# Optimization experiments

Measured on AMD Instinct MI355X. Metric: run time of the kernel, lower is better.

The kernel has to match this reference:

```python
import jax, jax.numpy as jnp
import numpy as np

N_RAYS = 8192
N_SAMPLES = 64   # timesteps per ray
HID = 128
BOOSTER = 1.0
FAR = 10.0


def rsh_cart_3(d):
    # real spherical harmonics, cartesian, degree 3 -> 16 coefficients
    x, y, z = d[..., 0], d[..., 1], d[..., 2]
    x2, y2, z2 = x * x, y * y, z * z
    return jnp.stack([
        jnp.full_like(x, 0.282094791773878),
        -0.488602511902920 * y,
        0.488602511902920 * z,
        -0.488602511902920 * x,
        1.092548430592079 * x * y,
        -1.092548430592079 * y * z,
        0.315391565252520 * (3.0 * z2 - 1.0),
        -1.092548430592079 * x * z,
        0.546274215296040 * (x2 - y2),
        -0.590043589926644 * y * (3.0 * x2 - y2),
        2.890611442640554 * x * y * z,
        -0.457045799464466 * y * (5.0 * z2 - 1.0),
        0.373176332590115 * z * (5.0 * z2 - 3.0),
        -0.457045799464466 * x * (5.0 * z2 - 1.0),
        1.445305721320277 * z * (x2 - y2),
        -0.590043589926644 * x * (x2 - 3.0 * y2),
    ], axis=-1)


def setup_inputs() -> dict:
    key = jax.random.key(0)
    ks = jax.random.split(key, 10)
    N, H = N_RAYS, HID

    def w(k, shape, fan_in):
        return (jax.random.normal(k, shape, jnp.float32) / np.float32(np.sqrt(fan_in)))

    return dict(
        rays_o=jax.random.normal(ks[0], (N, 3), jnp.float32) * 0.3,
        rays_d=jax.random.normal(ks[1], (N, 3), jnp.float32),
        aabb=jnp.array([[-1.0, -1.0, -1.0], [1.0, 1.0, 1.0]], jnp.float32),
        W1=w(ks[2], (3, H), 3), b1=jnp.zeros((H,), jnp.float32),
        W2=w(ks[3], (H, H), H), b2=jnp.zeros((H,), jnp.float32),
        Wd=w(ks[4], (H, 1), H), bd=jnp.zeros((1,), jnp.float32),
        Wf=w(ks[5], (H, 16), H), bf=jnp.zeros((16,), jnp.float32),
        Wc1=w(ks[6], (32, H), 32), bc1=jnp.zeros((H,), jnp.float32),
        Wc2=w(ks[7], (H, 3), H), bc2=jnp.zeros((3,), jnp.float32),
    )


def reference(rays_o, rays_d, aabb, W1, b1, W2, b2, Wd, bd, Wf, bf, Wc1, bc1, Wc2, bc2):
    # --- ray / AABB intersection (slab test), as in RayBundle.intersect_aabb ---
    inv_d = 1.0 / rays_d
    t1 = (aabb[0] - rays_o) * inv_d
    t2 = (aabb[1] - rays_o) * inv_d
    tnear = jnp.maximum(jnp.max(jnp.minimum(t1, t2), -1), 0.0)      # (N,)
    tfar = jnp.minimum(jnp.min(jnp.maximum(t1, t2), -1), FAR)       # (N,)
    active = tnear < tfar                                           # active_mask()
    tnear = jnp.where(active, tnear, 0.0)
    tfar = jnp.where(active, tfar, 1.0)

    # --- timestep sampler: midpoint stratification between tnear/tfar ---
    T = N_SAMPLES
    frac = (jnp.arange(T, dtype=rays_o.dtype) + 0.5) / T
    ts = tnear[:, None] + frac[None, :] * (tfar - tnear)[:, None]    # (N,T)
    xyz = rays_o[:, None, :] + rays_d[:, None, :] * ts[..., None]    # (N,T,3)

    # --- convert_world_to_box_normalized + BoundsFilter.test ---
    xyz_ndc = (xyz - aabb[0]) / (aabb[1] - aabb[0]) * 2.0 - 1.0
    inside = jnp.all((xyz_ndc >= -1.0) & (xyz_ndc <= 1.0), -1)       # (N,T)

    # --- direction harmonics (rsh_cart_3 of normalized direction) ---
    dnorm = jnp.linalg.norm(rays_d, axis=-1, keepdims=True)          # (N,1)
    ynm = rsh_cart_3(rays_d / dnorm)                                 # (N,16)

    # --- radiance field MLP (query-everywhere; masked points contribute 0) ---
    h = jax.nn.relu(xyz_ndc @ W1 + b1)
    h = jax.nn.relu(h @ W2 + b2)
    sigma = jnp.exp(h @ Wd + bd)[..., 0]                             # (N,T) density
    feat = h @ Wf + bf                                               # (N,T,16)
    cond = jnp.broadcast_to(ynm[:, None, :], feat.shape)
    hc = jax.nn.relu(jnp.concatenate([feat, cond], -1) @ Wc1 + bc1)
    color = jax.nn.sigmoid(hc @ Wc2 + bc2)                           # (N,T,3)
    m = inside.astype(sigma.dtype)
    sigma = sigma * m                                                # scatter-zeros equiv
    color = color * m[..., None]

    # --- integrate_timesteps: transmittance * alpha weights ---
    tfinal = tfar + BOOSTER
    deltas = jnp.concatenate([ts[:, 1:] - ts[:, :-1], tfinal[:, None] - ts[:, -1:]], -1)
    tau = sigma * deltas * dnorm                                     # (N,T)
    excl = jnp.concatenate([jnp.zeros_like(tau[:, :1]), jnp.cumsum(tau[:, :-1], -1)], -1)
    weights = jnp.exp(-excl) * (1.0 - jnp.exp(-tau))                 # (N,T)

    # --- color_map / alpha_map / depth_map ---
    cmap = jnp.einsum('nt,ntc->nc', weights, color)                  # (N,3)
    amap = jnp.sum(weights, -1, keepdims=True)                       # (N,1)
    dmap = jnp.sum(weights * ts, -1, keepdims=True)                  # (N,1)
    am = active[:, None].astype(cmap.dtype)
    return jnp.concatenate([cmap * am, amap * am, dmap * am], -1)    # (N,5)
```

## Files before the change

kernel.cpp:

```cpp
#include <hip/hip_runtime.h>
#include <math.h>

#define THREADS 512
#define GRID 512
#define NRAYS 8192
#define FAR_T 10.0f
#define CSTR 24

typedef __attribute__((ext_vector_type(8))) short short8;
typedef __attribute__((ext_vector_type(4))) float f32x4;

static __device__ __forceinline__ unsigned f2bfu(float f) {
    unsigned u = __builtin_bit_cast(unsigned, f);
    return (u + 0x7fffu + ((u >> 16) & 1u)) >> 16;
}
static __device__ __forceinline__ unsigned pk2(float a, float b) {
    unsigned ra = __builtin_bit_cast(unsigned, a) + 0x8000u;
    unsigned rb = __builtin_bit_cast(unsigned, b) + 0x8000u;
    return __builtin_amdgcn_perm(rb, ra, 0x07060302u);
}
static __device__ __forceinline__ int sw128(int r, int k) { return (r << 7) + (k ^ ((r & 7) << 3)); }
static __device__ __forceinline__ int sw32(int r, int k)  { return (r << 5) + (k ^ ((r & 3) << 3)); }
static __device__ __forceinline__ f32x4 MFMA16(short8 a, short8 b, f32x4 c) {
    return __builtin_amdgcn_mfma_f32_16x16x32_bf16(a, b, c, 0, 0, 0);
}

struct RayP { float ox,oy,oz,dx,dy,dz,tn,tf,tstep,dnorm; bool act; };

static __device__ __forceinline__ RayP raySetup(const float* __restrict__ ro, const float* __restrict__ rd,
        int r, float a0x,float a0y,float a0z,float a1x,float a1y,float a1z) {
    RayP R;
    R.ox=ro[3*r+0]; R.oy=ro[3*r+1]; R.oz=ro[3*r+2];
    R.dx=rd[3*r+0]; R.dy=rd[3*r+1]; R.dz=rd[3*r+2];
    float ivx=1.f/R.dx, ivy=1.f/R.dy, ivz=1.f/R.dz;
    float t1x=(a0x-R.ox)*ivx, t2x=(a1x-R.ox)*ivx;
    float t1y=(a0y-R.oy)*ivy, t2y=(a1y-R.oy)*ivy;
    float t1z=(a0z-R.oz)*ivz, t2z=(a1z-R.oz)*ivz;
    float tn = fmaxf(fmaxf(fminf(t1x,t2x),fminf(t1y,t2y)),fminf(t1z,t2z));
    tn = fmaxf(tn, 0.f);
    float tf = fminf(fminf(fmaxf(t1x,t2x),fmaxf(t1y,t2y)),fmaxf(t1z,t2z));
    tf = fminf(tf, FAR_T);
    R.act = tn < tf;
    R.tn = R.act ? tn : 0.f;
    R.tf = R.act ? tf : 1.f;
    R.tstep = (R.tf - R.tn) * (1.f/64.f);
    R.dnorm = sqrtf(R.dx*R.dx + R.dy*R.dy + R.dz*R.dz);
    return R;
}

__global__ __launch_bounds__(THREADS, 4)
void RadianceRenderer_kernel(const float* __restrict__ rays_o, const float* __restrict__ rays_d,
                             const float* __restrict__ aabb,
                             const float* __restrict__ W1, const float* __restrict__ b1,
                             const float* __restrict__ W2, const float* __restrict__ b2,
                             const float* __restrict__ Wd, const float* __restrict__ bd,
                             const float* __restrict__ Wf, const float* __restrict__ bf,
                             const float* __restrict__ Wc1, const float* __restrict__ bc1,
                             const float* __restrict__ Wc2, const float* __restrict__ bc2,
                             float* __restrict__ out)
{
    __shared__ __align__(16) short W1T[128*8];
    __shared__ __align__(16) short Wfd17[17*128];
    __shared__ __align__(16) short Wc2T3[3*128];
    __shared__ __align__(16) float B2F[128];
    __shared__ __align__(16) float BC1F[128];
    __shared__ __align__(16) union {
        struct { short W2T[128*128]; short Wc1T[128*32]; } w;
        struct { short H1[128*128]; short H2[128*128];
                 short CC[128*CSTR];
                 float CS[4*128]; } a;
    } sm;

    const int tid  = threadIdx.x;
    const int lane = tid & 63;
    const int wv   = tid >> 6;
    const int l15  = lane & 15;
    const int l4   = lane >> 4;
    const short8 z8 = {0,0,0,0,0,0,0,0};

    for (int i = tid; i < 128*128; i += THREADS) {
        int k = i >> 7, n = i & 127;
        sm.w.W2T[sw128(n, k)] = (short)f2bfu(W2[i]);
    }
    for (int i = tid; i < 128*32; i += THREADS) {
        int n = i >> 5, k = i & 31;
        sm.w.Wc1T[sw32(n, k)] = (short)f2bfu(Wc1[k*128 + n]);
    }
    for (int i = tid; i < 17*128; i += THREADS) {
        int n = i >> 7, k = i & 127;
        float v = (n < 16) ? Wf[k*16 + n] : Wd[k];
        Wfd17[sw128(n, k)] = (short)f2bfu(v);
    }
    for (int i = tid; i < 3*128; i += THREADS) {
        int c = i >> 7, k = i & 127;
        Wc2T3[i] = (short)f2bfu(Wc2[k*3 + c]);
    }
    for (int i = tid; i < 128*8; i += THREADS) {
        int ch = i >> 3, k = i & 7;
        float f = (k < 3) ? W1[k*128 + ch] : ((k == 3) ? b1[ch] : 0.f);
        W1T[i] = (short)f2bfu(f);
    }
    for (int i = tid; i < 128; i += THREADS) { B2F[i] = b2[i]; BC1F[i] = bc1[i]; }
    __syncthreads();

    const int chB = (wv >> 1) * 32;
    const int smB = (wv & 1) * 64;
    const int sB3 = wv * 16;

    short8 w2f[2][4], wc1f[2];
    #pragma unroll
    for (int jn = 0; jn < 2; ++jn)
        #pragma unroll
        for (int kk = 0; kk < 4; ++kk)
            w2f[jn][kk] = *(const short8*)&sm.w.W2T[sw128(chB + 16*jn + l15, kk*32 + 8*l4)];
    #pragma unroll
    for (int cg = 0; cg < 2; ++cg)
        wc1f[cg] = *(const short8*)&sm.w.Wc1T[sw32(chB + 16*cg + l15, 8*l4)];

    f32x4 bfv;
    #pragma unroll
    for (int vv = 0; vv < 4; ++vv) bfv[vv] = bf[4*l4 + vv];
    float bc2r[3] = { bc2[0], bc2[1], bc2[2] };
    const float bdr = bd[0];

    const float a0x=aabb[0],a0y=aabb[1],a0z=aabb[2],a1x=aabb[3],a1y=aabb[4],a1z=aabb[5];
    const float scx=2.f/(a1x-a0x), scy=2.f/(a1y-a0y), scz=2.f/(a1z-a0z);

    __syncthreads();

    for (int i = tid; i < 128*CSTR/2; i += THREADS) ((unsigned*)sm.a.CC)[i] = 0u;
    __syncthreads();

    int gp = -1;

    for (int g = blockIdx.x; g < NRAYS/2; g += gridDim.x) {
        if (wv == 4 || wv == 5) {
            const int m   = tid - 256;
            const int ray = 2*g + (m >> 6);
            RayP R = raySetup(rays_o, rays_d, ray, a0x,a0y,a0z,a1x,a1y,a1z);
            const int s = m & 63;
            float t  = R.tn + ((float)s + 0.5f) * R.tstep;
            float px = fmaf(R.dx, t, R.ox);
            float py = fmaf(R.dy, t, R.oy);
            float pz = fmaf(R.dz, t, R.oz);
            float nx = fmaf(px - a0x, scx, -1.f);
            float ny = fmaf(py - a0y, scy, -1.f);
            float nz = fmaf(pz - a0z, scz, -1.f);
            *(uint2*)&sm.a.CC[m*CSTR] = make_uint2(pk2(nx, ny), pk2(nz, 1.0f));
            if (s == 0) {
                float inorm = 1.f / R.dnorm;
                float x = R.dx*inorm, y = R.dy*inorm, z = R.dz*inorm;
                float x2 = x*x, y2 = y*y, z2 = z*z;
                unsigned q0 = pk2(0.282094791773878f,              -0.488602511902920f*y);
                unsigned q1 = pk2(0.488602511902920f*z,            -0.488602511902920f*x);
                unsigned q2 = pk2(1.092548430592079f*x*y,          -1.092548430592079f*y*z);
                unsigned q3 = pk2(0.315391565252520f*(3.f*z2-1.f), -1.092548430592079f*x*z);
                unsigned q4 = pk2(0.546274215296040f*(x2-y2),      -0.590043589926644f*y*(3.f*x2-y2));
                unsigned q5 = pk2(2.890611442640554f*x*y*z,        -0.457045799464466f*y*(5.f*z2-1.f));
                unsigned q6 = pk2(0.373176332590115f*z*(5.f*z2-3.f), -0.457045799464466f*x*(5.f*z2-1.f));
                unsigned q7 = pk2(1.445305721320277f*z*(x2-y2),    -0.590043589926644f*x*(x2-3.f*y2));
                *(uint4*)&sm.a.CC[m*CSTR + 16]        = make_uint4(q0,q1,q2,q3);
                *(uint4*)&sm.a.CC[(m+1)*CSTR + 16]    = make_uint4(q4,q5,q6,q7);
            }
        } else if (wv < 2 && gp >= 0) {
            RayP R = raySetup(rays_o, rays_d, 2*gp + wv, a0x,a0y,a0z,a1x,a1y,a1z);
            const int m = wv*64 + lane;
            float t  = R.tn + ((float)lane + 0.5f) * R.tstep;
            float px = fmaf(R.dx, t, R.ox);
            float py = fmaf(R.dy, t, R.oy);
            float pz = fmaf(R.dz, t, R.oz);
            float nx = fmaf(px - a0x, scx, -1.f);
            float ny = fmaf(py - a0y, scy, -1.f);
            float nz = fmaf(pz - a0z, scz, -1.f);
            bool ins = (nx >= -1.f) & (nx <= 1.f) & (ny >= -1.f) & (ny <= 1.f)
                     & (nz >= -1.f) & (nz <= 1.f);
            float sig = ins ? __expf(sm.a.CS[3*128 + m] + bdr) : 0.f;
            float delta = (lane == 63) ? (R.tf + 1.0f - t) : R.tstep;
            float tau = sig * delta * R.dnorm;
            float cum = tau;
            #pragma unroll
            for (int off = 1; off < 64; off <<= 1) {
                float tmp = __shfl_up(cum, off);
                if (lane >= off) cum += tmp;
            }
            float excl = cum - tau;
            float wgt = __expf(-excl) * (1.f - __expf(-tau));
            float c0 = wgt * sm.a.CS[0*128 + m];
            float c1 = wgt * sm.a.CS[1*128 + m];
            float c2 = wgt * sm.a.CS[2*128 + m];
            float amv = wgt;
            float dmv = wgt * t;
            #pragma unroll
            for (int off = 32; off; off >>= 1) {
                c0  += __shfl_xor(c0,  off);
                c1  += __shfl_xor(c1,  off);
                c2  += __shfl_xor(c2,  off);
                amv += __shfl_xor(amv, off);
                dmv += __shfl_xor(dmv, off);
            }
            if (lane == 0) {
                float msk = R.act ? 1.f : 0.f;
                int ray = 2*gp + wv;
                out[ray*5+0] = c0*msk;
                out[ray*5+1] = c1*msk;
                out[ray*5+2] = c2*msk;
                out[ray*5+3] = amv*msk;
                out[ray*5+4] = dmv*msk;
            }
        }
        __syncthreads();

        {
            short8 bx[4];
            #pragma unroll
            for (int im = 0; im < 4; ++im) {
                short8 v = z8;
                if (l4 == 0) v = *(const short8*)&sm.a.CC[(smB + 16*im + l15)*CSTR];
                bx[im] = v;
            }
            #pragma unroll
            for (int jn = 0; jn < 2; ++jn) {
                short8 w1fr = z8;
                if (l4 == 0) w1fr = *(const short8*)&W1T[(chB + 16*jn + l15)*8];
                #pragma unroll
                for (int im = 0; im < 4; ++im) {
                    f32x4 v = MFMA16(w1fr, bx[im], (f32x4){0.f,0.f,0.f,0.f});
                    int m  = smB + 16*im + l15;
                    int n0 = chB + 16*jn + 4*l4;
                    float r0 = fmaxf(v[0], 0.f), r1 = fmaxf(v[1], 0.f);
                    float r2 = fmaxf(v[2], 0.f), r3 = fmaxf(v[3], 0.f);
                    *(uint2*)&sm.a.H1[sw128(m, n0)] = make_uint2(pk2(r0,r1), pk2(r2,r3));
                }
            }
        }
        __syncthreads();

        {
            f32x4 acc[2][4];
            #pragma unroll
            for (int jn = 0; jn < 2; ++jn) {
                f32x4 bias = *(const f32x4*)&B2F[chB + 16*jn + 4*l4];
                #pragma unroll
                for (int im = 0; im < 4; ++im) acc[jn][im] = bias;
            }
            #pragma unroll
            for (int kk = 0; kk < 4; ++kk)
                #pragma unroll
                for (int im = 0; im < 4; ++im) {
                    short8 bfr = *(const short8*)&sm.a.H1[sw128(smB + 16*im + l15, kk*32 + 8*l4)];
                    acc[0][im] = MFMA16(w2f[0][kk], bfr, acc[0][im]);
                    acc[1][im] = MFMA16(w2f[1][kk], bfr, acc[1][im]);
                }
            #pragma unroll
            for (int jn = 0; jn < 2; ++jn)
                #pragma unroll
                for (int im = 0; im < 4; ++im) {
                    int m  = smB + 16*im + l15;
                    int n0 = chB + 16*jn + 4*l4;
                    f32x4 v = acc[jn][im];
                    float r0 = fmaxf(v[0], 0.f), r1 = fmaxf(v[1], 0.f);
                    float r2 = fmaxf(v[2], 0.f), r3 = fmaxf(v[3], 0.f);
                    *(uint2*)&sm.a.H2[sw128(m, n0)] = make_uint2(pk2(r0,r1), pk2(r2,r3));
                }
        }
        __syncthreads();

        {
            f32x4 f30 = bfv;
            f32x4 f31 = (f32x4){0.f,0.f,0.f,0.f};
            const int m = sB3 + l15;
            #pragma unroll
            for (int kk = 0; kk < 4; ++kk) {
                short8 bA = *(const short8*)&sm.a.H2[sw128(m, kk*32 + 8*l4)];
                short8 wfd0 = *(const short8*)&Wfd17[sw128(l15, kk*32 + 8*l4)];
                short8 wfd1 = z8;
                if (l15 == 0) wfd1 = *(const short8*)&Wfd17[sw128(16, kk*32 + 8*l4)];
                f30 = MFMA16(wfd0, bA, f30);
                f31 = MFMA16(wfd1, bA, f31);
            }
            *(uint2*)&sm.a.CC[m*CSTR + 4*l4] = make_uint2(pk2(f30[0],f30[1]), pk2(f30[2],f30[3]));
            if (l4 == 0) sm.a.CS[3*128 + m] = f31[0];
        }
        __syncthreads();

        {
            short8 bcc[4];
            #pragma unroll
            for (int sg = 0; sg < 4; ++sg) {
                int m = smB + 16*sg + l15;
                if (l4 < 2) bcc[sg] = *(const short8*)&sm.a.CC[m*CSTR + 8*l4];
                else        bcc[sg] = *(const short8*)&sm.a.CC[((m >> 6)*64 + (l4 - 2))*CSTR + 16];
            }
            #pragma unroll
            for (int cg = 0; cg < 2; ++cg) {
                f32x4 bias = *(const f32x4*)&BC1F[chB + 16*cg + 4*l4];
                #pragma unroll
                for (int sg = 0; sg < 4; ++sg) {
                    f32x4 v = MFMA16(wc1f[cg], bcc[sg], bias);
                    int m  = smB + 16*sg + l15;
                    int n0 = chB + 16*cg + 4*l4;
                    float r0 = fmaxf(v[0], 0.f), r1 = fmaxf(v[1], 0.f);
                    float r2 = fmaxf(v[2], 0.f), r3 = fmaxf(v[3], 0.f);
                    *(uint2*)&sm.a.H1[sw128(m, n0)] = make_uint2(pk2(r0,r1), pk2(r2,r3));
                }
            }
        }
        __syncthreads();

        {
            f32x4 c5 = (f32x4){0.f,0.f,0.f,0.f};
            const int m = sB3 + l15;
            #pragma unroll
            for (int kk = 0; kk < 4; ++kk) {
                short8 wc2fr = z8;
                if (l15 < 3) wc2fr = *(const short8*)&Wc2T3[l15*128 + kk*32 + 8*l4];
                short8 b = *(const short8*)&sm.a.H1[sw128(m, kk*32 + 8*l4)];
                c5 = MFMA16(wc2fr, b, c5);
            }
            if (l4 == 0) {
                #pragma unroll
                for (int vv = 0; vv < 3; ++vv)
                    sm.a.CS[vv*128 + m] = 1.f / (1.f + __expf(-(c5[vv] + bc2r[vv])));
            }
        }
        __syncthreads();

        gp = g;
    }

    if (gp >= 0 && wv < 2) {
        RayP R = raySetup(rays_o, rays_d, 2*gp + wv, a0x,a0y,a0z,a1x,a1y,a1z);
        const int m = wv*64 + lane;
        float t  = R.tn + ((float)lane + 0.5f) * R.tstep;
        float px = fmaf(R.dx, t, R.ox);
        float py = fmaf(R.dy, t, R.oy);
        float pz = fmaf(R.dz, t, R.oz);
        float nx = fmaf(px - a0x, scx, -1.f);
        float ny = fmaf(py - a0y, scy, -1.f);
        float nz = fmaf(pz - a0z, scz, -1.f);
        bool ins = (nx >= -1.f) & (nx <= 1.f) & (ny >= -1.f) & (ny <= 1.f)
                 & (nz >= -1.f) & (nz <= 1.f);
        float sig = ins ? __expf(sm.a.CS[3*128 + m] + bdr) : 0.f;
        float delta = (lane == 63) ? (R.tf + 1.0f - t) : R.tstep;
        float tau = sig * delta * R.dnorm;
        float cum = tau;
        #pragma unroll
        for (int off = 1; off < 64; off <<= 1) {
            float tmp = __shfl_up(cum, off);
            if (lane >= off) cum += tmp;
        }
        float excl = cum - tau;
        float wgt = __expf(-excl) * (1.f - __expf(-tau));
        float c0 = wgt * sm.a.CS[0*128 + m];
        float c1 = wgt * sm.a.CS[1*128 + m];
        float c2 = wgt * sm.a.CS[2*128 + m];
        float amv = wgt;
        float dmv = wgt * t;
        #pragma unroll
        for (int off = 32; off; off >>= 1) {
            c0  += __shfl_xor(c0,  off);
            c1  += __shfl_xor(c1,  off);
            c2  += __shfl_xor(c2,  off);
            amv += __shfl_xor(amv, off);
            dmv += __shfl_xor(dmv, off);
        }
        if (lane == 0) {
            float msk = R.act ? 1.f : 0.f;
            int ray = 2*gp + wv;
            out[ray*5+0] = c0*msk;
            out[ray*5+1] = c1*msk;
            out[ray*5+2] = c2*msk;
            out[ray*5+3] = amv*msk;
            out[ray*5+4] = dmv*msk;
        }
    }
}

extern "C" void kernel_launch(void* const* d_in, const int* in_sizes, int n_in,
                              void* d_out, int out_size, void* d_ws, size_t ws_size,
                              hipStream_t stream) {
    (void)in_sizes; (void)n_in; (void)d_ws; (void)ws_size; (void)out_size;
    const float* rays_o = (const float*)d_in[0];
    const float* rays_d = (const float*)d_in[1];
    const float* aabb   = (const float*)d_in[2];
    const float* W1  = (const float*)d_in[3];
    const float* b1  = (const float*)d_in[4];
    const float* W2  = (const float*)d_in[5];
    const float* b2  = (const float*)d_in[6];
    const float* Wd  = (const float*)d_in[7];
    const float* bd  = (const float*)d_in[8];
    const float* Wf  = (const float*)d_in[9];
    const float* bf  = (const float*)d_in[10];
    const float* Wc1 = (const float*)d_in[11];
    const float* bc1 = (const float*)d_in[12];
    const float* Wc2 = (const float*)d_in[13];
    const float* bc2 = (const float*)d_in[14];
    float* out = (float*)d_out;

    hipLaunchKernelGGL(RadianceRenderer_kernel, dim3(GRID), dim3(THREADS), 0, stream,
                       rays_o, rays_d, aabb, W1, b1, W2, b2, Wd, bd,
                       Wf, bf, Wc1, bc1, Wc2, bc2, out);
}
```

Before: 147.9 us.

## Give each wave its own 16 samples to drop block-wide barriers

```diff
diff --git a/kernel.cpp b/kernel.cpp
--- a/kernel.cpp
+++ b/kernel.cpp
@@ -5,7 +5,6 @@
 #define GRID 512
 #define NRAYS 8192
 #define FAR_T 10.0f
-#define CSTR 24
 
 typedef __attribute__((ext_vector_type(8))) short short8;
 typedef __attribute__((ext_vector_type(4))) float f32x4;
@@ -59,17 +58,15 @@
                              const float* __restrict__ Wc2, const float* __restrict__ bc2,
                              float* __restrict__ out)
 {
-    __shared__ __align__(16) short W1T[128*8];
-    __shared__ __align__(16) short Wfd17[17*128];
-    __shared__ __align__(16) short Wc2T3[3*128];
-    __shared__ __align__(16) float B2F[128];
-    __shared__ __align__(16) float BC1F[128];
-    __shared__ __align__(16) union {
-        struct { short W2T[128*128]; short Wc1T[128*32]; } w;
-        struct { short H1[128*128]; short H2[128*128];
-                 short CC[128*CSTR];
-                 float CS[4*128]; } a;
-    } sm;
+    __shared__ __align__(16) short W2T[16384];
+    __shared__ __align__(16) short Wc1T[4096];
+    __shared__ __align__(16) short WfdT[2176];
+    __shared__ __align__(16) short Wc2T3[384];
+    __shared__ __align__(16) short W1T[1024];
+    __shared__ __align__(16) short B2H[128], BC1H[128];
+    __shared__ __align__(16) short HS[8*2048];
+    __shared__ float WS[8];
+    __shared__ float WP[8][5];
 
     const int tid  = threadIdx.x;
     const int lane = tid & 63;
@@ -78,49 +75,41 @@
     const int l4   = lane >> 4;
     const short8 z8 = {0,0,0,0,0,0,0,0};
 
-    for (int i = tid; i < 128*128; i += THREADS) {
+    for (int i = tid; i < 16384; i += THREADS) {
         int k = i >> 7, n = i & 127;
-        sm.w.W2T[sw128(n, k)] = (short)f2bfu(W2[i]);
-    }
-    for (int i = tid; i < 128*32; i += THREADS) {
+        W2T[sw128(n, k)] = (short)f2bfu(W2[i]);
+    }
+    for (int i = tid; i < 4096; i += THREADS) {
         int n = i >> 5, k = i & 31;
-        sm.w.Wc1T[sw32(n, k)] = (short)f2bfu(Wc1[k*128 + n]);
-    }
-    for (int i = tid; i < 17*128; i += THREADS) {
+        Wc1T[sw32(n, k)] = (short)f2bfu(Wc1[k*128 + n]);
+    }
+    for (int i = tid; i < 2176; i += THREADS) {
         int n = i >> 7, k = i & 127;
         float v = (n < 16) ? Wf[k*16 + n] : Wd[k];
-        Wfd17[sw128(n, k)] = (short)f2bfu(v);
-    }
-    for (int i = tid; i < 3*128; i += THREADS) {
+        WfdT[sw128(n, k)] = (short)f2bfu(v);
+    }
+    for (int i = tid; i < 384; i += THREADS) {
         int c = i >> 7, k = i & 127;
         Wc2T3[i] = (short)f2bfu(Wc2[k*3 + c]);
     }
-    for (int i = tid; i < 128*8; i += THREADS) {
+    for (int i = tid; i < 1024; i += THREADS) {
         int ch = i >> 3, k = i & 7;
         float f = (k < 3) ? W1[k*128 + ch] : ((k == 3) ? b1[ch] : 0.f);
         W1T[i] = (short)f2bfu(f);
     }
-    for (int i = tid; i < 128; i += THREADS) { B2F[i] = b2[i]; BC1F[i] = bc1[i]; }
-    __syncthreads();
-
-    const int chB = (wv >> 1) * 32;
-    const int smB = (wv & 1) * 64;
-    const int sB3 = wv * 16;
-
-    short8 w2f[2][4], wc1f[2];
-    #pragma unroll
-    for (int jn = 0; jn < 2; ++jn)
-        #pragma unroll
-        for (int kk = 0; kk < 4; ++kk)
-            w2f[jn][kk] = *(const short8*)&sm.w.W2T[sw128(chB + 16*jn + l15, kk*32 + 8*l4)];
-    #pragma unroll
-    for (int cg = 0; cg < 2; ++cg)
-        wc1f[cg] = *(const short8*)&sm.w.Wc1T[sw32(chB + 16*cg + l15, 8*l4)];
+    for (int i = tid; i < 128; i += THREADS) {
+        B2H[i]  = (short)f2bfu(b2[i]);
+        BC1H[i] = (short)f2bfu(bc1[i]);
+    }
+
+    const int rayOff = wv >> 2;
+    const int sb     = (wv & 3) * 16;
+    const int hsB    = wv * 2048;
 
     f32x4 bfv;
     #pragma unroll
     for (int vv = 0; vv < 4; ++vv) bfv[vv] = bf[4*l4 + vv];
-    float bc2r[3] = { bc2[0], bc2[1], bc2[2] };
+    const float bc2r0 = bc2[0], bc2r1 = bc2[1], bc2r2 = bc2[2];
     const float bdr = bd[0];
 
     const float a0x=aabb[0],a0y=aabb[1],a0z=aabb[2],a1x=aabb[3],a1y=aabb[4],a1z=aabb[5];
@@ -128,250 +117,180 @@
 
     __syncthreads();
 
-    for (int i = tid; i < 128*CSTR/2; i += THREADS) ((unsigned*)sm.a.CC)[i] = 0u;
-    __syncthreads();
-
-    int gp = -1;
-
     for (int g = blockIdx.x; g < NRAYS/2; g += gridDim.x) {
-        if (wv == 4 || wv == 5) {
-            const int m   = tid - 256;
-            const int ray = 2*g + (m >> 6);
-            RayP R = raySetup(rays_o, rays_d, ray, a0x,a0y,a0z,a1x,a1y,a1z);
-            const int s = m & 63;
-            float t  = R.tn + ((float)s + 0.5f) * R.tstep;
-            float px = fmaf(R.dx, t, R.ox);
-            float py = fmaf(R.dy, t, R.oy);
-            float pz = fmaf(R.dz, t, R.oz);
-            float nx = fmaf(px - a0x, scx, -1.f);
-            float ny = fmaf(py - a0y, scy, -1.f);
-            float nz = fmaf(pz - a0z, scz, -1.f);
-            *(uint2*)&sm.a.CC[m*CSTR] = make_uint2(pk2(nx, ny), pk2(nz, 1.0f));
-            if (s == 0) {
-                float inorm = 1.f / R.dnorm;
-                float x = R.dx*inorm, y = R.dy*inorm, z = R.dz*inorm;
-                float x2 = x*x, y2 = y*y, z2 = z*z;
-                unsigned q0 = pk2(0.282094791773878f,              -0.488602511902920f*y);
-                unsigned q1 = pk2(0.488602511902920f*z,            -0.488602511902920f*x);
-                unsigned q2 = pk2(1.092548430592079f*x*y,          -1.092548430592079f*y*z);
-                unsigned q3 = pk2(0.315391565252520f*(3.f*z2-1.f), -1.092548430592079f*x*z);
-                unsigned q4 = pk2(0.546274215296040f*(x2-y2),      -0.590043589926644f*y*(3.f*x2-y2));
-                unsigned q5 = pk2(2.890611442640554f*x*y*z,        -0.457045799464466f*y*(5.f*z2-1.f));
-                unsigned q6 = pk2(0.373176332590115f*z*(5.f*z2-3.f), -0.457045799464466f*x*(5.f*z2-1.f));
-                unsigned q7 = pk2(1.445305721320277f*z*(x2-y2),    -0.590043589926644f*x*(x2-3.f*y2));
-                *(uint4*)&sm.a.CC[m*CSTR + 16]        = make_uint4(q0,q1,q2,q3);
-                *(uint4*)&sm.a.CC[(m+1)*CSTR + 16]    = make_uint4(q4,q5,q6,q7);
-            }
-        } else if (wv < 2 && gp >= 0) {
-            RayP R = raySetup(rays_o, rays_d, 2*gp + wv, a0x,a0y,a0z,a1x,a1y,a1z);
-            const int m = wv*64 + lane;
-            float t  = R.tn + ((float)lane + 0.5f) * R.tstep;
-            float px = fmaf(R.dx, t, R.ox);
-            float py = fmaf(R.dy, t, R.oy);
-            float pz = fmaf(R.dz, t, R.oz);
-            float nx = fmaf(px - a0x, scx, -1.f);
-            float ny = fmaf(py - a0y, scy, -1.f);
-            float nz = fmaf(pz - a0z, scz, -1.f);
-            bool ins = (nx >= -1.f) & (nx <= 1.f) & (ny >= -1.f) & (ny <= 1.f)
-                     & (nz >= -1.f) & (nz <= 1.f);
-            float sig = ins ? __expf(sm.a.CS[3*128 + m] + bdr) : 0.f;
-            float delta = (lane == 63) ? (R.tf + 1.0f - t) : R.tstep;
-            float tau = sig * delta * R.dnorm;
-            float cum = tau;
-            #pragma unroll
-            for (int off = 1; off < 64; off <<= 1) {
-                float tmp = __shfl_up(cum, off);
-                if (lane >= off) cum += tmp;
-            }
-            float excl = cum - tau;
-            float wgt = __expf(-excl) * (1.f - __expf(-tau));
-            float c0 = wgt * sm.a.CS[0*128 + m];
-            float c1 = wgt * sm.a.CS[1*128 + m];
-            float c2 = wgt * sm.a.CS[2*128 + m];
-            float amv = wgt;
-            float dmv = wgt * t;
-            #pragma unroll
-            for (int off = 32; off; off >>= 1) {
-                c0  += __shfl_xor(c0,  off);
-                c1  += __shfl_xor(c1,  off);
-                c2  += __shfl_xor(c2,  off);
-                amv += __shfl_xor(amv, off);
-                dmv += __shfl_xor(dmv, off);
-            }
-            if (lane == 0) {
-                float msk = R.act ? 1.f : 0.f;
-                int ray = 2*gp + wv;
-                out[ray*5+0] = c0*msk;
-                out[ray*5+1] = c1*msk;
-                out[ray*5+2] = c2*msk;
-                out[ray*5+3] = amv*msk;
-                out[ray*5+4] = dmv*msk;
-            }
-        }
-        __syncthreads();
-
-        {
-            short8 bx[4];
-            #pragma unroll
-            for (int im = 0; im < 4; ++im) {
-                short8 v = z8;
-                if (l4 == 0) v = *(const short8*)&sm.a.CC[(smB + 16*im + l15)*CSTR];
-                bx[im] = v;
-            }
-            #pragma unroll
-            for (int jn = 0; jn < 2; ++jn) {
-                short8 w1fr = z8;
-                if (l4 == 0) w1fr = *(const short8*)&W1T[(chB + 16*jn + l15)*8];
+        const int ray = 2*g + rayOff;
+        const RayP R = raySetup(rays_o, rays_d, ray, a0x,a0y,a0z,a1x,a1y,a1z);
+
+        const int s = sb + l15;
+        const float t  = R.tn + ((float)s + 0.5f) * R.tstep;
+        const float px = fmaf(R.dx, t, R.ox);
+        const float py = fmaf(R.dy, t, R.oy);
+        const float pz = fmaf(R.dz, t, R.oz);
+        const float nx = fmaf(px - a0x, scx, -1.f);
+        const float ny = fmaf(py - a0y, scy, -1.f);
+        const float nz = fmaf(pz - a0z, scz, -1.f);
+        const bool ins = (nx >= -1.f) & (nx <= 1.f) & (ny >= -1.f) & (ny <= 1.f)
+                       & (nz >= -1.f) & (nz <= 1.f);
+
+        short8 ybf;
+        {
+            float inorm = 1.f / R.dnorm;
+            float x = R.dx*inorm, y = R.dy*inorm, z = R.dz*inorm;
+            float x2=x*x, y2=y*y, z2=z*z;
+            float y0 = 0.282094791773878f;
+            float y1 = -0.488602511902920f*y;
+            float y2v= 0.488602511902920f*z;
+            float y3 = -0.488602511902920f*x;
+            float y4 = 1.092548430592079f*x*y;
+            float y5 = -1.092548430592079f*y*z;
+            float y6 = 0.315391565252520f*(3.f*z2-1.f);
+            float y7 = -1.092548430592079f*x*z;
+            float y8 = 0.546274215296040f*(x2-y2);
+            float y9 = -0.590043589926644f*y*(3.f*x2-y2);
+            float y10= 2.890611442640554f*x*y*z;
+            float y11= -0.457045799464466f*y*(5.f*z2-1.f);
+            float y12= 0.373176332590115f*z*(5.f*z2-3.f);
+            float y13= -0.457045799464466f*x*(5.f*z2-1.f);
+            float y14= 1.445305721320277f*z*(x2-y2);
+            float y15= -0.590043589926644f*x*(x2-3.f*y2);
+            bool hi = (l4 == 3);
+            uint4 q = { pk2(hi?y8 :y0 , hi?y9 :y1 ),
+                        pk2(hi?y10:y2v, hi?y11:y3 ),
+                        pk2(hi?y12:y4 , hi?y13:y5 ),
+                        pk2(hi?y14:y6 , hi?y15:y7 ) };
+            ybf = __builtin_bit_cast(short8, q);
+        }
+
+        {
+            short8 bx = z8;
+            if (l4 == 0) {
+                uint4 q = { pk2(nx, ny), pk2(nz, 1.0f), 0u, 0u };
+                bx = __builtin_bit_cast(short8, q);
+            }
+            #pragma unroll
+            for (int t8 = 0; t8 < 8; ++t8) {
+                short8 a = z8;
+                if (l4 == 0) a = *(const short8*)&W1T[(t8*16 + l15)*8];
+                f32x4 d = MFMA16(a, bx, (f32x4){0.f,0.f,0.f,0.f});
+                float r0 = fmaxf(d[0],0.f), r1 = fmaxf(d[1],0.f);
+                float r2 = fmaxf(d[2],0.f), r3 = fmaxf(d[3],0.f);
+                *(uint2*)&HS[hsB + sw128(l15, t8*16 + 4*l4)] = make_uint2(pk2(r0,r1), pk2(r2,r3));
+            }
+        }
+
+        {
+            short8 kb[4];
+            #pragma unroll
+            for (int kk = 0; kk < 4; ++kk)
+                kb[kk] = *(const short8*)&HS[hsB + sw128(l15, kk*32 + 8*l4)];
+            #pragma unroll
+            for (int t8 = 0; t8 < 8; ++t8) {
+                uint2 bu = *(const uint2*)&B2H[t8*16 + 4*l4];
+                f32x4 acc = { __builtin_bit_cast(float, bu.x << 16),
+                              __builtin_bit_cast(float, bu.x & 0xffff0000u),
+                              __builtin_bit_cast(float, bu.y << 16),
+                              __builtin_bit_cast(float, bu.y & 0xffff0000u) };
                 #pragma unroll
-                for (int im = 0; im < 4; ++im) {
-                    f32x4 v = MFMA16(w1fr, bx[im], (f32x4){0.f,0.f,0.f,0.f});
-                    int m  = smB + 16*im + l15;
-                    int n0 = chB + 16*jn + 4*l4;
-                    float r0 = fmaxf(v[0], 0.f), r1 = fmaxf(v[1], 0.f);
-                    float r2 = fmaxf(v[2], 0.f), r3 = fmaxf(v[3], 0.f);
-                    *(uint2*)&sm.a.H1[sw128(m, n0)] = make_uint2(pk2(r0,r1), pk2(r2,r3));
+                for (int kk = 0; kk < 4; ++kk) {
+                    short8 a = *(const short8*)&W2T[sw128(t8*16 + l15, kk*32 + 8*l4)];
+                    acc = MFMA16(a, kb[kk], acc);
                 }
-            }
-        }
-        __syncthreads();
-
-        {
-            f32x4 acc[2][4];
-            #pragma unroll
-            for (int jn = 0; jn < 2; ++jn) {
-                f32x4 bias = *(const f32x4*)&B2F[chB + 16*jn + 4*l4];
-                #pragma unroll
-                for (int im = 0; im < 4; ++im) acc[jn][im] = bias;
-            }
+                float r0 = fmaxf(acc[0],0.f), r1 = fmaxf(acc[1],0.f);
+                float r2 = fmaxf(acc[2],0.f), r3 = fmaxf(acc[3],0.f);
+                *(uint2*)&HS[hsB + sw128(l15, t8*16 + 4*l4)] = make_uint2(pk2(r0,r1), pk2(r2,r3));
+            }
+        }
+
+        float sigdot;
+        {
+            short8 kb[4];
             #pragma unroll
             for (int kk = 0; kk < 4; ++kk)
-                #pragma unroll
-                for (int im = 0; im < 4; ++im) {
-                    short8 bfr = *(const short8*)&sm.a.H1[sw128(smB + 16*im + l15, kk*32 + 8*l4)];
-                    acc[0][im] = MFMA16(w2f[0][kk], bfr, acc[0][im]);
-                    acc[1][im] = MFMA16(w2f[1][kk], bfr, acc[1][im]);
-                }
-            #pragma unroll
-            for (int jn = 0; jn < 2; ++jn)
-                #pragma unroll
-                for (int im = 0; im < 4; ++im) {
-                    int m  = smB + 16*im + l15;
-                    int n0 = chB + 16*jn + 4*l4;
-                    f32x4 v = acc[jn][im];
-                    float r0 = fmaxf(v[0], 0.f), r1 = fmaxf(v[1], 0.f);
-                    float r2 = fmaxf(v[2], 0.f), r3 = fmaxf(v[3], 0.f);
-                    *(uint2*)&sm.a.H2[sw128(m, n0)] = make_uint2(pk2(r0,r1), pk2(r2,r3));
-                }
-        }
-        __syncthreads();
-
-        {
+                kb[kk] = *(const short8*)&HS[hsB + sw128(l15, kk*32 + 8*l4)];
             f32x4 f30 = bfv;
             f32x4 f31 = (f32x4){0.f,0.f,0.f,0.f};
-            const int m = sB3 + l15;
             #pragma unroll
             for (int kk = 0; kk < 4; ++kk) {
-                short8 bA = *(const short8*)&sm.a.H2[sw128(m, kk*32 + 8*l4)];
-                short8 wfd0 = *(const short8*)&Wfd17[sw128(l15, kk*32 + 8*l4)];
-                short8 wfd1 = z8;
-                if (l15 == 0) wfd1 = *(const short8*)&Wfd17[sw128(16, kk*32 + 8*l4)];
-                f30 = MFMA16(wfd0, bA, f30);
-                f31 = MFMA16(wfd1, bA, f31);
-            }
-            *(uint2*)&sm.a.CC[m*CSTR + 4*l4] = make_uint2(pk2(f30[0],f30[1]), pk2(f30[2],f30[3]));
-            if (l4 == 0) sm.a.CS[3*128 + m] = f31[0];
-        }
-        __syncthreads();
-
-        {
-            short8 bcc[4];
-            #pragma unroll
-            for (int sg = 0; sg < 4; ++sg) {
-                int m = smB + 16*sg + l15;
-                if (l4 < 2) bcc[sg] = *(const short8*)&sm.a.CC[m*CSTR + 8*l4];
-                else        bcc[sg] = *(const short8*)&sm.a.CC[((m >> 6)*64 + (l4 - 2))*CSTR + 16];
-            }
-            #pragma unroll
-            for (int cg = 0; cg < 2; ++cg) {
-                f32x4 bias = *(const f32x4*)&BC1F[chB + 16*cg + 4*l4];
-                #pragma unroll
-                for (int sg = 0; sg < 4; ++sg) {
-                    f32x4 v = MFMA16(wc1f[cg], bcc[sg], bias);
-                    int m  = smB + 16*sg + l15;
-                    int n0 = chB + 16*cg + 4*l4;
-                    float r0 = fmaxf(v[0], 0.f), r1 = fmaxf(v[1], 0.f);
-                    float r2 = fmaxf(v[2], 0.f), r3 = fmaxf(v[3], 0.f);
-                    *(uint2*)&sm.a.H1[sw128(m, n0)] = make_uint2(pk2(r0,r1), pk2(r2,r3));
-                }
-            }
-        }
-        __syncthreads();
-
-        {
-            f32x4 c5 = (f32x4){0.f,0.f,0.f,0.f};
-            const int m = sB3 + l15;
+                short8 a0 = *(const short8*)&WfdT[sw128(l15, kk*32 + 8*l4)];
+                short8 a1 = z8;
+                if (l15 == 0) a1 = *(const short8*)&WfdT[sw128(16, kk*32 + 8*l4)];
+                f30 = MFMA16(a0, kb[kk], f30);
+                f31 = MFMA16(a1, kb[kk], f31);
+            }
+            sigdot = f31[0];
+            *(uint2*)&HS[hsB + sw128(l15, 4*l4)] = make_uint2(pk2(f30[0],f30[1]), pk2(f30[2],f30[3]));
+        }
+
+        {
+            short8 bg;
+            if (l4 < 2) bg = *(const short8*)&HS[hsB + sw128(l15, 8*l4)];
+            else        bg = ybf;
+            #pragma unroll
+            for (int t8 = 0; t8 < 8; ++t8) {
+                uint2 bu = *(const uint2*)&BC1H[t8*16 + 4*l4];
+                f32x4 acc = { __builtin_bit_cast(float, bu.x << 16),
+                              __builtin_bit_cast(float, bu.x & 0xffff0000u),
+                              __builtin_bit_cast(float, bu.y << 16),
+                              __builtin_bit_cast(float, bu.y & 0xffff0000u) };
+                short8 a = *(const short8*)&Wc1T[sw32(t8*16 + l15, 8*l4)];
+                f32x4 v = MFMA16(a, bg, acc);
+                float r0 = fmaxf(v[0],0.f), r1 = fmaxf(v[1],0.f);
+                float r2 = fmaxf(v[2],0.f), r3 = fmaxf(v[3],0.f);
+                *(uint2*)&HS[hsB + sw128(l15, t8*16 + 4*l4)] = make_uint2(pk2(r0,r1), pk2(r2,r3));
+            }
+        }
+
+        f32x4 c5 = (f32x4){0.f,0.f,0.f,0.f};
+        {
             #pragma unroll
             for (int kk = 0; kk < 4; ++kk) {
-                short8 wc2fr = z8;
-                if (l15 < 3) wc2fr = *(const short8*)&Wc2T3[l15*128 + kk*32 + 8*l4];
-                short8 b = *(const short8*)&sm.a.H1[sw128(m, kk*32 + 8*l4)];
-                c5 = MFMA16(wc2fr, b, c5);
-            }
-            if (l4 == 0) {
-                #pragma unroll
-                for (int vv = 0; vv < 3; ++vv)
-                    sm.a.CS[vv*128 + m] = 1.f / (1.f + __expf(-(c5[vv] + bc2r[vv])));
-            }
-        }
-        __syncthreads();
-
-        gp = g;
-    }
-
-    if (gp >= 0 && wv < 2) {
-        RayP R = raySetup(rays_o, rays_d, 2*gp + wv, a0x,a0y,a0z,a1x,a1y,a1z);
-        const int m = wv*64 + lane;
-        float t  = R.tn + ((float)lane + 0.5f) * R.tstep;
-        float px = fmaf(R.dx, t, R.ox);
-        float py = fmaf(R.dy, t, R.oy);
-        float pz = fmaf(R.dz, t, R.oz);
-        float nx = fmaf(px - a0x, scx, -1.f);
-        float ny = fmaf(py - a0y, scy, -1.f);
-        float nz = fmaf(pz - a0z, scz, -1.f);
-        bool ins = (nx >= -1.f) & (nx <= 1.f) & (ny >= -1.f) & (ny <= 1.f)
-                 & (nz >= -1.f) & (nz <= 1.f);
-        float sig = ins ? __expf(sm.a.CS[3*128 + m] + bdr) : 0.f;
-        float delta = (lane == 63) ? (R.tf + 1.0f - t) : R.tstep;
-        float tau = sig * delta * R.dnorm;
+                short8 a = z8;
+                if (l15 < 3) a = *(const short8*)&Wc2T3[l15*128 + kk*32 + 8*l4];
+                short8 b = *(const short8*)&HS[hsB + sw128(l15, kk*32 + 8*l4)];
+                c5 = MFMA16(a, b, c5);
+            }
+        }
+        const float cr = 1.f / (1.f + __expf(-(c5[0] + bc2r0)));
+        const float cg = 1.f / (1.f + __expf(-(c5[1] + bc2r1)));
+        const float cb = 1.f / (1.f + __expf(-(c5[2] + bc2r2)));
+
+        const float sig = ins ? __expf(sigdot + bdr) : 0.f;
+        const float delta = (s == 63) ? (R.tf + 1.0f - t) : R.tstep;
+        const float tau = sig * delta * R.dnorm;
         float cum = tau;
         #pragma unroll
-        for (int off = 1; off < 64; off <<= 1) {
+        for (int off = 1; off < 16; off <<= 1) {
             float tmp = __shfl_up(cum, off);
-            if (lane >= off) cum += tmp;
-        }
-        float excl = cum - tau;
-        float wgt = __expf(-excl) * (1.f - __expf(-tau));
-        float c0 = wgt * sm.a.CS[0*128 + m];
-        float c1 = wgt * sm.a.CS[1*128 + m];
-        float c2 = wgt * sm.a.CS[2*128 + m];
-        float amv = wgt;
-        float dmv = wgt * t;
+            if ((lane & 15) >= off) cum += tmp;
+        }
+        const float sumtau = __shfl(cum, 15);
+        if (lane == 0) WS[wv] = sumtau;
+        __syncthreads();
+        float prev = 0.f;
+        {
+            int wb = wv & 4, wq = wv & 3;
+            if (wq > 0) prev += WS[wb+0];
+            if (wq > 1) prev += WS[wb+1];
+            if (wq > 2) prev += WS[wb+2];
+        }
+        const float excl = prev + cum - tau;
+        const float wgt = __expf(-excl) * (1.f - __expf(-tau));
+        float p0 = wgt*cr, p1 = wgt*cg, p2 = wgt*cb, p3 = wgt, p4 = wgt*t;
         #pragma unroll
-        for (int off = 32; off; off >>= 1) {
-            c0  += __shfl_xor(c0,  off);
-            c1  += __shfl_xor(c1,  off);
-            c2  += __shfl_xor(c2,  off);
-            amv += __shfl_xor(amv, off);
-            dmv += __shfl_xor(dmv, off);
+        for (int off = 1; off < 16; off <<= 1) {
+            p0 += __shfl_xor(p0, off);
+            p1 += __shfl_xor(p1, off);
+            p2 += __shfl_xor(p2, off);
+            p3 += __shfl_xor(p3, off);
+            p4 += __shfl_xor(p4, off);
         }
         if (lane == 0) {
-            float msk = R.act ? 1.f : 0.f;
-            int ray = 2*gp + wv;
-            out[ray*5+0] = c0*msk;
-            out[ray*5+1] = c1*msk;
-            out[ray*5+2] = c2*msk;
-            out[ray*5+3] = amv*msk;
-            out[ray*5+4] = dmv*msk;
+            WP[wv][0]=p0; WP[wv][1]=p1; WP[wv][2]=p2; WP[wv][3]=p3; WP[wv][4]=p4;
+        }
+        __syncthreads();
+        if ((wv & 3) == 0 && lane < 5) {
+            float v = WP[wv][lane] + WP[wv+1][lane] + WP[wv+2][lane] + WP[wv+3][lane];
+            out[ray*5 + lane] = v * (R.act ? 1.f : 0.f);
         }
     }
 }
```

Measured after the change: 160.3 us. 8.4% more time.
